# Performance work log

Hardware: AMD Instinct MI355X
Metric: run time of the kernel (lower is better)

Reference implementation:

```python
import jax, jax.numpy as jnp
import numpy as np

DIM = 1024
EPS = 1e-5

def layernorm(x, g, b):
    m = jnp.mean(x, axis=-1, keepdims=True)
    v = jnp.var(x, axis=-1, keepdims=True)
    return (x - m) / jnp.sqrt(v + EPS) * g + b

def setup_inputs() -> dict:
    key = jax.random.key(0)
    ks = jax.random.split(key, 12)
    B, L, D = 4, 2048, DIM
    s = 1.0 / np.sqrt(D)
    return {
        "q": jax.random.normal(ks[0], (B, L, D), jnp.float32),
        "k": jax.random.normal(ks[1], (B, L, D), jnp.float32),
        "v": jax.random.normal(ks[2], (B, L, D), jnp.float32),
        "gq": jnp.ones((D,), jnp.float32), "bq": jnp.zeros((D,), jnp.float32),
        "gk": jnp.ones((D,), jnp.float32), "bk": jnp.zeros((D,), jnp.float32),
        "gv": jnp.ones((D,), jnp.float32), "bv": jnp.zeros((D,), jnp.float32),
        "Wq": jax.random.uniform(ks[3], (D, D), jnp.float32, -s, s),
        "Wk": jax.random.uniform(ks[4], (D, D), jnp.float32, -s, s),
        "Wv": jax.random.uniform(ks[5], (D, D), jnp.float32, -s, s),
        "Wp": jax.random.uniform(ks[6], (D, D), jnp.float32, -s, s),
        "bp": jax.random.uniform(ks[7], (D,), jnp.float32, -s, s),
    }

def reference(q, k, v, gq, bq, gk, bk, gv, bv, Wq, Wk, Wv, Wp, bp):
    scale = DIM ** -0.5
    qn = layernorm(q, gq, bq) @ Wq.T  # [B,Q,D]
    kn = layernorm(k, gk, bk) @ Wk.T  # [B,K,D]
    vn = layernorm(v, gv, bv) @ Wv.T  # [B,K,D]
    attn = jnp.einsum('bqc,bkc->bqk', qn, kn)
    attn = jax.nn.relu(attn) * scale  # ReLU on raw scores, then scale (matches in-place *=)
    attn_mask = jax.nn.softmax(attn, axis=-1)
    out = jnp.einsum('bqk,bkc->bqc', attn_mask, vn)
    out = out @ Wp.T + bp
    return (attn, out)
```

## Files before the change

kernel.cpp:

```cpp
#include <hip/hip_runtime.h>


typedef __attribute__((ext_vector_type(8))) short short8v;
typedef __attribute__((ext_vector_type(4))) float f32x4;

#define DEVI __device__ __forceinline__

DEVI float b2f(unsigned short u) {
  union { unsigned int i; float f; } x;
  x.i = ((unsigned int)u) << 16;
  return x.f;
}
DEVI unsigned short f2b(float f) {
  union { float f; unsigned int i; } x;
  x.f = f;
  unsigned int r = x.i + 0x7fffu + ((x.i >> 16) & 1u);
  return (unsigned short)(r >> 16);
}

DEVI bool sniff_bf16(const unsigned short* wq) {
  int bad = 0;
#pragma unroll
  for (int j = 0; j < 64; ++j) bad |= (fabsf(b2f(wq[j])) > 0.0625f) ? 1 : 0;
  return bad == 0;
}

DEVI void async16(const unsigned short* g, unsigned short* l) {
  __builtin_amdgcn_global_load_lds(
      (const __attribute__((address_space(1))) void*)g,
      (__attribute__((address_space(3))) void*)l, 16, 0, 0);
}

DEVI void wait_lgkm0() { asm volatile("s_waitcnt lgkmcnt(0)" ::: "memory"); }
template <int N> DEVI void wait_vm();
template <> DEVI void wait_vm<0>() { asm volatile("s_waitcnt vmcnt(0)" ::: "memory"); }
template <> DEVI void wait_vm<2>() { asm volatile("s_waitcnt vmcnt(2)" ::: "memory"); }

DEVI void stage_half(const unsigned short* G, int ld, unsigned short* L,
                     int w, int lane, int k0) {
  int r8 = lane >> 3;
  int scol = ((lane & 7) ^ r8) * 8;
#pragma unroll
  for (int j = 0; j < 2; ++j) {
    async16(G + (size_t)(j * 64 + w * 8 + r8) * ld + k0 + scol,
            L + (j * 64 + w * 8) * 64);
  }
}

DEVI void gemm8_core(unsigned short* sA, unsigned short* sB,
                     const unsigned short* Ab, const unsigned short* Bb,
                     int m0, int n0, int lda, int ldb, int K, int tid,
                     f32x4 (&acc)[8][4]) {
  int lane = tid & 63, w = tid >> 6;
  int wm = w >> 2, wn = w & 3;
  int l15 = lane & 15, quad = lane >> 4;
  int rxor = l15 & 7;
  int cb0 = (quad ^ rxor) * 8;
  int cb1 = ((4 + quad) ^ rxor) * 8;
  const int nst = K >> 6;
  const unsigned short* A0 = Ab + (size_t)m0 * lda;
  const unsigned short* A1 = A0 + (size_t)128 * lda;
  const unsigned short* B0 = Bb + (size_t)n0 * ldb;
  const unsigned short* B1 = B0 + (size_t)128 * ldb;

  stage_half(A0, lda, sA, w, lane, 0);
  stage_half(A1, lda, sA + 8192, w, lane, 0);
  stage_half(B0, ldb, sB, w, lane, 0);
  stage_half(B1, ldb, sB + 8192, w, lane, 0);

  for (int t = 0; t < nst; ++t) {
    const int b = t & 1, nb2 = b ^ 1;
    const bool st = (t + 1 < nst);
    const int k0n = (t + 1) << 6;
    const unsigned short* rA = sA + b * 16384 + (wm * 128 + l15) * 64;
    const unsigned short* rB = sB + b * 16384 + (wn * 64 + l15) * 64;
    short8v a[4][2], bb[4][2];

    if (st) {
      stage_half(A0, lda, sA + nb2 * 16384, w, lane, k0n);
      wait_vm<2>();
    } else {
      wait_vm<0>();
    }
    __builtin_amdgcn_s_barrier();
#pragma unroll
    for (int mt = 0; mt < 4; ++mt) {
      a[mt][0] = *(const short8v*)(rA + mt * 1024 + cb0);
      a[mt][1] = *(const short8v*)(rA + mt * 1024 + cb1);
    }
#pragma unroll
    for (int nt = 0; nt < 2; ++nt) {
      bb[nt][0] = *(const short8v*)(rB + nt * 1024 + cb0);
      bb[nt][1] = *(const short8v*)(rB + nt * 1024 + cb1);
    }
    wait_lgkm0();
    __builtin_amdgcn_sched_barrier(0);
    __builtin_amdgcn_s_setprio(1);
#pragma unroll
    for (int mt = 0; mt < 4; ++mt)
#pragma unroll
      for (int nt = 0; nt < 2; ++nt) {
        acc[mt][nt] = __builtin_amdgcn_mfma_f32_16x16x32_bf16(a[mt][0], bb[nt][0], acc[mt][nt], 0, 0, 0);
        acc[mt][nt] = __builtin_amdgcn_mfma_f32_16x16x32_bf16(a[mt][1], bb[nt][1], acc[mt][nt], 0, 0, 0);
      }
    __builtin_amdgcn_s_setprio(0);
    __builtin_amdgcn_s_barrier();

#pragma unroll
    for (int nt = 2; nt < 4; ++nt) {
      bb[nt][0] = *(const short8v*)(rB + nt * 1024 + cb0);
      bb[nt][1] = *(const short8v*)(rB + nt * 1024 + cb1);
    }
    if (st) stage_half(A1, lda, sA + nb2 * 16384 + 8192, w, lane, k0n);
    __builtin_amdgcn_s_barrier();
    wait_lgkm0();
    __builtin_amdgcn_sched_barrier(0);
    __builtin_amdgcn_s_setprio(1);
#pragma unroll
    for (int mt = 0; mt < 4; ++mt)
#pragma unroll
      for (int nt = 2; nt < 4; ++nt) {
        acc[mt][nt] = __builtin_amdgcn_mfma_f32_16x16x32_bf16(a[mt][0], bb[nt][0], acc[mt][nt], 0, 0, 0);
        acc[mt][nt] = __builtin_amdgcn_mfma_f32_16x16x32_bf16(a[mt][1], bb[nt][1], acc[mt][nt], 0, 0, 0);
      }
    __builtin_amdgcn_s_setprio(0);
    __builtin_amdgcn_s_barrier();

#pragma unroll
    for (int mt = 0; mt < 4; ++mt) {
      a[mt][0] = *(const short8v*)(rA + (4 + mt) * 1024 + cb0);
      a[mt][1] = *(const short8v*)(rA + (4 + mt) * 1024 + cb1);
    }
    if (st) stage_half(B0, ldb, sB + nb2 * 16384, w, lane, k0n);
    __builtin_amdgcn_s_barrier();
    wait_lgkm0();
    __builtin_amdgcn_sched_barrier(0);
    __builtin_amdgcn_s_setprio(1);
#pragma unroll
    for (int mt = 0; mt < 4; ++mt)
#pragma unroll
      for (int nt = 0; nt < 2; ++nt) {
        acc[4 + mt][nt] = __builtin_amdgcn_mfma_f32_16x16x32_bf16(a[mt][0], bb[nt][0], acc[4 + mt][nt], 0, 0, 0);
        acc[4 + mt][nt] = __builtin_amdgcn_mfma_f32_16x16x32_bf16(a[mt][1], bb[nt][1], acc[4 + mt][nt], 0, 0, 0);
      }
    __builtin_amdgcn_s_setprio(0);
    __builtin_amdgcn_s_barrier();

    if (st) stage_half(B1, ldb, sB + nb2 * 16384 + 8192, w, lane, k0n);
    __builtin_amdgcn_s_barrier();
    __builtin_amdgcn_s_setprio(1);
#pragma unroll
    for (int mt = 0; mt < 4; ++mt)
#pragma unroll
      for (int nt = 2; nt < 4; ++nt) {
        acc[4 + mt][nt] = __builtin_amdgcn_mfma_f32_16x16x32_bf16(a[mt][0], bb[nt][0], acc[4 + mt][nt], 0, 0, 0);
        acc[4 + mt][nt] = __builtin_amdgcn_mfma_f32_16x16x32_bf16(a[mt][1], bb[nt][1], acc[4 + mt][nt], 0, 0, 0);
      }
    __builtin_amdgcn_s_setprio(0);
    __builtin_amdgcn_s_barrier();
  }
}

DEVI int xcd_swz(int f, int nb) { return (f & 7) * (nb >> 3) + (f >> 3); }

struct PrepArgs {
  const void* q; const void* k; const void* v;
  const void* g[3]; const void* b[3];
  const void* W[4];
};

__global__ __launch_bounds__(256) void k_prep(PrepArgs pa,
    unsigned short* __restrict__ Wb, unsigned short* __restrict__ XN) {
  bool isbf = sniff_bf16((const unsigned short*)pa.W[0]);
  int bid = blockIdx.x, tid = threadIdx.x;
  if (bid < 2048) {
    int s = bid >> 9;
    size_t inner = ((size_t)(bid & 511)) * 2048 + (size_t)tid * 8;
    unsigned short* dst = Wb + (size_t)s * 1048576 + inner;
    if (isbf) {
      *(uint4*)dst = *(const uint4*)((const unsigned short*)pa.W[s] + inner);
    } else {
      const float* f = (const float*)pa.W[s] + inner;
      float4 a = *(const float4*)f;
      float4 b = *(const float4*)(f + 4);
      ushort4 o0 = { f2b(a.x), f2b(a.y), f2b(a.z), f2b(a.w) };
      ushort4 o1 = { f2b(b.x), f2b(b.y), f2b(b.z), f2b(b.w) };
      *(ushort4*)dst = o0;
      *(ushort4*)(dst + 4) = o1;
    }
  } else {
    int row = bid - 2048;
    int t = row >> 13;
    size_t r = (size_t)(row & 8191);
    const void* src = (t == 0) ? pa.q : (t == 1) ? pa.k : pa.v;
    float x0, x1, x2, x3;
    if (isbf) {
      ushort4 pk = *(const ushort4*)((const unsigned short*)src + r * 1024 + (size_t)tid * 4);
      x0 = b2f(pk.x); x1 = b2f(pk.y); x2 = b2f(pk.z); x3 = b2f(pk.w);
    } else {
      float4 pk = *(const float4*)((const float*)src + r * 1024 + (size_t)tid * 4);
      x0 = pk.x; x1 = pk.y; x2 = pk.z; x3 = pk.w;
    }
    float s1 = x0 + x1 + x2 + x3;
    float s2 = x0 * x0 + x1 * x1 + x2 * x2 + x3 * x3;
    for (int off = 32; off > 0; off >>= 1) {
      s1 += __shfl_down(s1, off);
      s2 += __shfl_down(s2, off);
    }
    __shared__ float sh[8];
    if ((tid & 63) == 0) { sh[tid >> 6] = s1; sh[4 + (tid >> 6)] = s2; }
    __syncthreads();
    float m  = (sh[0] + sh[1] + sh[2] + sh[3]) * (1.0f / 1024.0f);
    float m2 = (sh[4] + sh[5] + sh[6] + sh[7]) * (1.0f / 1024.0f);
    float rstd = rsqrtf(m2 - m * m + 1e-5f);
    float g0, g1, g2, g3, c0, c1, c2, c3;
    if (isbf) {
      ushort4 gv = *(const ushort4*)((const unsigned short*)pa.g[t] + tid * 4);
      ushort4 bbv = *(const ushort4*)((const unsigned short*)pa.b[t] + tid * 4);
      g0 = b2f(gv.x); g1 = b2f(gv.y); g2 = b2f(gv.z); g3 = b2f(gv.w);
      c0 = b2f(bbv.x); c1 = b2f(bbv.y); c2 = b2f(bbv.z); c3 = b2f(bbv.w);
    } else {
      float4 gv = *(const float4*)((const float*)pa.g[t] + tid * 4);
      float4 bbv = *(const float4*)((const float*)pa.b[t] + tid * 4);
      g0 = gv.x; g1 = gv.y; g2 = gv.z; g3 = gv.w;
      c0 = bbv.x; c1 = bbv.y; c2 = bbv.z; c3 = bbv.w;
    }
    ushort4 o;
    o.x = f2b((x0 - m) * rstd * g0 + c0);
    o.y = f2b((x1 - m) * rstd * g1 + c1);
    o.z = f2b((x2 - m) * rstd * g2 + c2);
    o.w = f2b((x3 - m) * rstd * g3 + c3);
    *(ushort4*)(XN + (size_t)row * 1024 + (size_t)tid * 4) = o;
  }
}

__global__ __launch_bounds__(512, 2) void k_megaproj(
    const unsigned short* __restrict__ XN, const unsigned short* __restrict__ Wb,
    unsigned short* __restrict__ QN, unsigned short* __restrict__ VNT) {
  __shared__ __align__(16) unsigned short sA[2 * 256 * 64];
  __shared__ __align__(16) unsigned short sB[2 * 256 * 64];
  int x = xcd_swz((int)blockIdx.x, 384), tid = threadIdx.x;
  int lane = tid & 63, w = tid >> 6;
  int wm = w >> 2, wn = w & 3;
  int l15 = lane & 15, quad = lane >> 4;
  f32x4 acc[8][4];
#pragma unroll
  for (int i = 0; i < 8; ++i)
#pragma unroll
    for (int j = 0; j < 4; ++j) acc[i][j] = (f32x4){0.f, 0.f, 0.f, 0.f};

  unsigned short* C;
  int m0, n0, ldc;
  if (x < 256) {
    int t = x >> 7, i = x & 127;
    m0 = (i >> 2) * 256; n0 = (i & 3) * 256; ldc = 1024;
    gemm8_core(sA, sB, XN + (size_t)t * 8388608, Wb + (size_t)t * 1048576,
               m0, n0, 1024, 1024, 1024, tid, acc);
    C = QN + (size_t)t * 8388608;
  } else {
    int i = x - 256, z = i >> 5, j = i & 31;
    m0 = (j >> 3) * 256; n0 = (j & 7) * 256; ldc = 2048;
    gemm8_core(sA, sB, Wb + 2 * 1048576, XN + 2 * 8388608 + (size_t)z * 2097152,
               m0, n0, 1024, 1024, 1024, tid, acc);
    C = VNT + (size_t)z * 2097152;
  }
#pragma unroll
  for (int mt = 0; mt < 8; ++mt) {
    int mb = m0 + wm * 128 + mt * 16 + quad * 4;
#pragma unroll
    for (int nt = 0; nt < 4; ++nt) {
      int n = n0 + wn * 64 + nt * 16 + l15;
      f32x4 vc = acc[mt][nt];
#pragma unroll
      for (int r2 = 0; r2 < 4; ++r2) C[(size_t)(mb + r2) * ldc + n] = f2b(vc[r2]);
    }
  }
}

template <int EPI>
__global__ __launch_bounds__(512, 2) void k_gemm(
    const unsigned short* __restrict__ A, const unsigned short* __restrict__ B,
    void* __restrict__ Cv, long long coff,
    int K, int lda, int ldb, int ldc,
    long long sAb, long long sBb, long long sCb,
    float scale, const void* __restrict__ bias,
    const unsigned short* __restrict__ wq_sniff) {
  __shared__ __align__(16) unsigned short sA[2 * 256 * 64];
  __shared__ __align__(16) unsigned short sB[2 * 256 * 64];
  int tid = threadIdx.x;
  int lane = tid & 63, w = tid >> 6;
  int wm = w >> 2, wn = w & 3;
  int l15 = lane & 15, quad = lane >> 4;

  int gx = gridDim.x, gy = gridDim.y;
  int nb = gx * gy * (int)gridDim.z;
  int f = (int)blockIdx.x + gx * ((int)blockIdx.y + gy * (int)blockIdx.z);
  f = xcd_swz(f, nb);
  int bx = f % gx;
  int rem = f / gx;
  int by = rem % gy;
  int bz = rem / gy;

  int m0 = by * 256, n0 = bx * 256;
  f32x4 acc[8][4];
#pragma unroll
  for (int i = 0; i < 8; ++i)
#pragma unroll
    for (int j = 0; j < 4; ++j) acc[i][j] = (f32x4){0.f, 0.f, 0.f, 0.f};

  gemm8_core(sA, sB, A + (long long)bz * sAb, B + (long long)bz * sBb,
             m0, n0, lda, ldb, K, tid, acc);

  long long cbase = coff + (long long)bz * sCb;
  bool isbf = (EPI != 0) ? sniff_bf16(wq_sniff) : true;
#pragma unroll
  for (int mt = 0; mt < 8; ++mt) {
    int mb = m0 + wm * 128 + mt * 16 + quad * 4;
#pragma unroll
    for (int nt = 0; nt < 4; ++nt) {
      int n = n0 + wn * 64 + nt * 16 + l15;
      f32x4 vc = acc[mt][nt];
      if (EPI == 0) {
        unsigned short* C = (unsigned short*)Cv + cbase;
#pragma unroll
        for (int r2 = 0; r2 < 4; ++r2) C[(size_t)(mb + r2) * ldc + n] = f2b(vc[r2]);
      } else if (EPI == 1) {
        if (isbf) {
          unsigned short* C = (unsigned short*)Cv + cbase;
#pragma unroll
          for (int r2 = 0; r2 < 4; ++r2)
            C[(size_t)(mb + r2) * ldc + n] = f2b(fmaxf(vc[r2], 0.f) * scale);
        } else {
          float* C = (float*)Cv + cbase;
#pragma unroll
          for (int r2 = 0; r2 < 4; ++r2)
            C[(size_t)(mb + r2) * ldc + n] = fmaxf(vc[r2], 0.f) * scale;
        }
      } else {
        float bv2 = isbf ? b2f(((const unsigned short*)bias)[n])
                         : ((const float*)bias)[n];
        if (isbf) {
          unsigned short* C = (unsigned short*)Cv + cbase;
#pragma unroll
          for (int r2 = 0; r2 < 4; ++r2) C[(size_t)(mb + r2) * ldc + n] = f2b(vc[r2] + bv2);
        } else {
          float* C = (float*)Cv + cbase;
#pragma unroll
          for (int r2 = 0; r2 < 4; ++r2) C[(size_t)(mb + r2) * ldc + n] = vc[r2] + bv2;
        }
      }
    }
  }
}

__global__ __launch_bounds__(256) void k_softmax(const void* __restrict__ S,
    unsigned short* __restrict__ P, const unsigned short* __restrict__ wq_sniff) {
  bool isbf = sniff_bf16(wq_sniff);
  size_t row = blockIdx.x;
  int tid = threadIdx.x;
  float v[8];
  if (isbf) {
    const unsigned short* s = (const unsigned short*)S + row * 2048 + (size_t)tid * 8;
    ushort4 a = *(const ushort4*)s;
    ushort4 b = *(const ushort4*)(s + 4);
    v[0] = b2f(a.x); v[1] = b2f(a.y); v[2] = b2f(a.z); v[3] = b2f(a.w);
    v[4] = b2f(b.x); v[5] = b2f(b.y); v[6] = b2f(b.z); v[7] = b2f(b.w);
  } else {
    const float* s = (const float*)S + row * 2048 + (size_t)tid * 8;
    float4 a = *(const float4*)s;
    float4 b = *(const float4*)(s + 4);
    v[0] = a.x; v[1] = a.y; v[2] = a.z; v[3] = a.w;
    v[4] = b.x; v[5] = b.y; v[6] = b.z; v[7] = b.w;
  }
  float mx = v[0];
#pragma unroll
  for (int j = 1; j < 8; ++j) mx = fmaxf(mx, v[j]);
  for (int off = 32; off > 0; off >>= 1) mx = fmaxf(mx, __shfl_down(mx, off));
  __shared__ float sh[8];
  if ((tid & 63) == 0) sh[tid >> 6] = mx;
  __syncthreads();
  mx = fmaxf(fmaxf(sh[0], sh[1]), fmaxf(sh[2], sh[3]));
  float sum = 0.f;
#pragma unroll
  for (int j = 0; j < 8; ++j) { v[j] = __expf(v[j] - mx); sum += v[j]; }
  for (int off = 32; off > 0; off >>= 1) sum += __shfl_down(sum, off);
  if ((tid & 63) == 0) sh[4 + (tid >> 6)] = sum;
  __syncthreads();
  float inv = 1.0f / (sh[4] + sh[5] + sh[6] + sh[7]);
  ushort4 o0 = { f2b(v[0] * inv), f2b(v[1] * inv), f2b(v[2] * inv), f2b(v[3] * inv) };
  ushort4 o1 = { f2b(v[4] * inv), f2b(v[5] * inv), f2b(v[6] * inv), f2b(v[7] * inv) };
  unsigned short* p = P + row * 2048 + (size_t)tid * 8;
  *(ushort4*)p = o0;
  *(ushort4*)(p + 4) = o1;
}

static const size_t MB_ = 1024 * 1024;
static const size_t OFF_W   = 0;
static const size_t OFF_XN  = 8 * MB_ + 128 * 1024;
static const size_t OFF_QN  = OFF_XN + 48 * MB_;
static const size_t OFF_VNT = OFF_QN + 32 * MB_;
static const size_t OFF_P   = OFF_XN;
static const size_t OFF_O1  = OFF_XN + 32 * MB_;

extern "C" void kernel_launch(void* const* d_in, const int* in_sizes, int n_in,
                              void* d_out, int out_size, void* d_ws, size_t ws_size,
                              hipStream_t stream) {
  (void)in_sizes; (void)n_in; (void)out_size; (void)ws_size;
  char* ws = (char*)d_ws;
  unsigned short* Wb  = (unsigned short*)(ws + OFF_W);
  unsigned short* XN  = (unsigned short*)(ws + OFF_XN);
  unsigned short* QN  = (unsigned short*)(ws + OFF_QN);
  unsigned short* VNT = (unsigned short*)(ws + OFF_VNT);
  unsigned short* P   = (unsigned short*)(ws + OFF_P);
  unsigned short* O1  = (unsigned short*)(ws + OFF_O1);
  const unsigned short* WqS = (const unsigned short*)d_in[9];

  PrepArgs pa;
  pa.q = d_in[0]; pa.k = d_in[1]; pa.v = d_in[2];
  pa.g[0] = d_in[3]; pa.b[0] = d_in[4];
  pa.g[1] = d_in[5]; pa.b[1] = d_in[6];
  pa.g[2] = d_in[7]; pa.b[2] = d_in[8];
  pa.W[0] = d_in[9]; pa.W[1] = d_in[10]; pa.W[2] = d_in[11]; pa.W[3] = d_in[12];

  k_prep<<<26624, 256, 0, stream>>>(pa, Wb, XN);

  k_megaproj<<<384, 512, 0, stream>>>(XN, Wb, QN, VNT);

  k_gemm<1><<<dim3(8, 8, 4), 512, 0, stream>>>(
      QN, QN + 8388608, d_out,
      0,
      1024, 1024, 1024, 2048,
      2097152LL, 2097152LL, 4194304LL,
      0.03125f, nullptr, WqS);

  k_softmax<<<8192, 256, 0, stream>>>(d_out, P, WqS);

  k_gemm<0><<<dim3(4, 8, 4), 512, 0, stream>>>(
      P, VNT, O1,
      0,
      2048, 2048, 2048, 1024,
      4194304LL, 2097152LL, 2097152LL,
      0.f, nullptr, WqS);

  k_gemm<3><<<dim3(4, 32, 1), 512, 0, stream>>>(
      O1, Wb + 3 * 1048576, d_out,
      16777216,
      1024, 1024, 1024, 1024,
      0LL, 0LL, 0LL,
      0.f, d_in[13], WqS);
}
```

Baseline: 461.5 us.

## Deepen GEMM prefetch pipeline and add narrow 256x128 tile variant

Templates the shared GEMM core on tile width. The 256x256 path now prefetches A two k-steps ahead and B one step ahead, issuing the loads at different points in the iteration so more global-to-LDS traffic overlaps the MFMA work. A new 256x128 path halves the N tile for the P·V and output-projection GEMMs, doubling their grid to 256 blocks so more CUs are occupied. The cost is more repeated reads of A across N tiles and tighter vmcnt bookkeeping that must match the number of loads in flight.

```diff
diff --git a/kernel.cpp b/kernel.cpp
--- a/kernel.cpp
+++ b/kernel.cpp
@@ -34,23 +34,26 @@
 DEVI void wait_lgkm0() { asm volatile("s_waitcnt lgkmcnt(0)" ::: "memory"); }
 template <int N> DEVI void wait_vm();
 template <> DEVI void wait_vm<0>() { asm volatile("s_waitcnt vmcnt(0)" ::: "memory"); }
-template <> DEVI void wait_vm<2>() { asm volatile("s_waitcnt vmcnt(2)" ::: "memory"); }
-
+template <> DEVI void wait_vm<6>() { asm volatile("s_waitcnt vmcnt(6)" ::: "memory"); }
+template <> DEVI void wait_vm<8>() { asm volatile("s_waitcnt vmcnt(8)" ::: "memory"); }
+
+DEVI void stage_q(const unsigned short* G, int ld, unsigned short* L,
+                  int w, int lane, int k0) {
+  int r8 = lane >> 3;
+  int scol = ((lane & 7) ^ r8) * 8;
+  async16(G + (size_t)(w * 8 + r8) * ld + k0 + scol, L + (w * 8) * 64);
+}
 DEVI void stage_half(const unsigned short* G, int ld, unsigned short* L,
                      int w, int lane, int k0) {
-  int r8 = lane >> 3;
-  int scol = ((lane & 7) ^ r8) * 8;
-#pragma unroll
-  for (int j = 0; j < 2; ++j) {
-    async16(G + (size_t)(j * 64 + w * 8 + r8) * ld + k0 + scol,
-            L + (j * 64 + w * 8) * 64);
-  }
-}
-
+  stage_q(G, ld, L, w, lane, k0);
+  stage_q(G + (size_t)64 * ld, ld, L + 64 * 64, w, lane, k0);
+}
+
+template <int NB>
 DEVI void gemm8_core(unsigned short* sA, unsigned short* sB,
                      const unsigned short* Ab, const unsigned short* Bb,
                      int m0, int n0, int lda, int ldb, int K, int tid,
-                     f32x4 (&acc)[8][4]) {
+                     f32x4 (&acc)[8][2 * NB]) {
   int lane = tid & 63, w = tid >> 6;
   int wm = w >> 2, wn = w & 3;
   int l15 = lane & 15, quad = lane >> 4;
@@ -58,106 +61,178 @@
   int cb0 = (quad ^ rxor) * 8;
   int cb1 = ((4 + quad) ^ rxor) * 8;
   const int nst = K >> 6;
-  const unsigned short* A0 = Ab + (size_t)m0 * lda;
-  const unsigned short* A1 = A0 + (size_t)128 * lda;
-  const unsigned short* B0 = Bb + (size_t)n0 * ldb;
-  const unsigned short* B1 = B0 + (size_t)128 * ldb;
-
-  stage_half(A0, lda, sA, w, lane, 0);
-  stage_half(A1, lda, sA + 8192, w, lane, 0);
-  stage_half(B0, ldb, sB, w, lane, 0);
-  stage_half(B1, ldb, sB + 8192, w, lane, 0);
-
-  for (int t = 0; t < nst; ++t) {
-    const int b = t & 1, nb2 = b ^ 1;
-    const bool st = (t + 1 < nst);
-    const int k0n = (t + 1) << 6;
-    const unsigned short* rA = sA + b * 16384 + (wm * 128 + l15) * 64;
-    const unsigned short* rB = sB + b * 16384 + (wn * 64 + l15) * 64;
-    short8v a[4][2], bb[4][2];
-
-    if (st) {
-      stage_half(A0, lda, sA + nb2 * 16384, w, lane, k0n);
-      wait_vm<2>();
-    } else {
-      wait_vm<0>();
-    }
-    __builtin_amdgcn_s_barrier();
-#pragma unroll
-    for (int mt = 0; mt < 4; ++mt) {
-      a[mt][0] = *(const short8v*)(rA + mt * 1024 + cb0);
-      a[mt][1] = *(const short8v*)(rA + mt * 1024 + cb1);
-    }
-#pragma unroll
-    for (int nt = 0; nt < 2; ++nt) {
-      bb[nt][0] = *(const short8v*)(rB + nt * 1024 + cb0);
-      bb[nt][1] = *(const short8v*)(rB + nt * 1024 + cb1);
-    }
-    wait_lgkm0();
-    __builtin_amdgcn_sched_barrier(0);
-    __builtin_amdgcn_s_setprio(1);
-#pragma unroll
-    for (int mt = 0; mt < 4; ++mt)
+  const int BSZ = NB * 128 * 64;
+  const unsigned short* A_ = Ab + (size_t)m0 * lda;
+  const unsigned short* B_ = Bb + (size_t)n0 * ldb;
+
+  if constexpr (NB == 2) {
+    stage_half(A_, lda, sA, w, lane, 0);
+    stage_half(A_ + (size_t)128 * lda, lda, sA + 8192, w, lane, 0);
+    stage_half(B_, ldb, sB, w, lane, 0);
+    stage_half(B_ + (size_t)128 * ldb, ldb, sB + 8192, w, lane, 0);
+    if (nst > 1) {
+      stage_half(A_, lda, sA + 16384, w, lane, 64);
+      stage_half(A_ + (size_t)128 * lda, lda, sA + 16384 + 8192, w, lane, 64);
+    }
+    for (int t = 0; t < nst; ++t) {
+      const int b = t & 1;
+      const unsigned short* rA = sA + b * 16384 + (wm * 128 + l15) * 64;
+      const unsigned short* rB = sB + b * 16384 + (wn * 64 + l15) * 64;
+      short8v a[4][2], bb[4][2];
+      if (t + 1 < nst) {
+        int kn = (t + 1) << 6;
+        stage_half(B_, ldb, sB + (b ^ 1) * 16384, w, lane, kn);
+        stage_half(B_ + (size_t)128 * ldb, ldb, sB + (b ^ 1) * 16384 + 8192, w, lane, kn);
+        wait_vm<8>();
+      } else {
+        wait_vm<0>();
+      }
+      __builtin_amdgcn_s_barrier();
+#pragma unroll
+      for (int mt = 0; mt < 4; ++mt) {
+        a[mt][0] = *(const short8v*)(rA + mt * 1024 + cb0);
+        a[mt][1] = *(const short8v*)(rA + mt * 1024 + cb1);
+      }
 #pragma unroll
       for (int nt = 0; nt < 2; ++nt) {
-        acc[mt][nt] = __builtin_amdgcn_mfma_f32_16x16x32_bf16(a[mt][0], bb[nt][0], acc[mt][nt], 0, 0, 0);
-        acc[mt][nt] = __builtin_amdgcn_mfma_f32_16x16x32_bf16(a[mt][1], bb[nt][1], acc[mt][nt], 0, 0, 0);
-      }
-    __builtin_amdgcn_s_setprio(0);
-    __builtin_amdgcn_s_barrier();
-
-#pragma unroll
-    for (int nt = 2; nt < 4; ++nt) {
-      bb[nt][0] = *(const short8v*)(rB + nt * 1024 + cb0);
-      bb[nt][1] = *(const short8v*)(rB + nt * 1024 + cb1);
-    }
-    if (st) stage_half(A1, lda, sA + nb2 * 16384 + 8192, w, lane, k0n);
-    __builtin_amdgcn_s_barrier();
-    wait_lgkm0();
-    __builtin_amdgcn_sched_barrier(0);
-    __builtin_amdgcn_s_setprio(1);
-#pragma unroll
-    for (int mt = 0; mt < 4; ++mt)
+        bb[nt][0] = *(const short8v*)(rB + nt * 1024 + cb0);
+        bb[nt][1] = *(const short8v*)(rB + nt * 1024 + cb1);
+      }
+      wait_lgkm0();
+      __builtin_amdgcn_sched_barrier(0);
+      __builtin_amdgcn_s_setprio(1);
+#pragma unroll
+      for (int mt = 0; mt < 4; ++mt)
+#pragma unroll
+        for (int nt = 0; nt < 2; ++nt) {
+          acc[mt][nt] = __builtin_amdgcn_mfma_f32_16x16x32_bf16(a[mt][0], bb[nt][0], acc[mt][nt], 0, 0, 0);
+          acc[mt][nt] = __builtin_amdgcn_mfma_f32_16x16x32_bf16(a[mt][1], bb[nt][1], acc[mt][nt], 0, 0, 0);
+        }
+      __builtin_amdgcn_s_setprio(0);
+      __builtin_amdgcn_s_barrier();
 #pragma unroll
       for (int nt = 2; nt < 4; ++nt) {
-        acc[mt][nt] = __builtin_amdgcn_mfma_f32_16x16x32_bf16(a[mt][0], bb[nt][0], acc[mt][nt], 0, 0, 0);
-        acc[mt][nt] = __builtin_amdgcn_mfma_f32_16x16x32_bf16(a[mt][1], bb[nt][1], acc[mt][nt], 0, 0, 0);
-      }
-    __builtin_amdgcn_s_setprio(0);
-    __builtin_amdgcn_s_barrier();
-
-#pragma unroll
-    for (int mt = 0; mt < 4; ++mt) {
-      a[mt][0] = *(const short8v*)(rA + (4 + mt) * 1024 + cb0);
-      a[mt][1] = *(const short8v*)(rA + (4 + mt) * 1024 + cb1);
-    }
-    if (st) stage_half(B0, ldb, sB + nb2 * 16384, w, lane, k0n);
-    __builtin_amdgcn_s_barrier();
-    wait_lgkm0();
-    __builtin_amdgcn_sched_barrier(0);
-    __builtin_amdgcn_s_setprio(1);
-#pragma unroll
-    for (int mt = 0; mt < 4; ++mt)
+        bb[nt][0] = *(const short8v*)(rB + nt * 1024 + cb0);
+        bb[nt][1] = *(const short8v*)(rB + nt * 1024 + cb1);
+      }
+      __builtin_amdgcn_s_barrier();
+      wait_lgkm0();
+      __builtin_amdgcn_sched_barrier(0);
+      __builtin_amdgcn_s_setprio(1);
+#pragma unroll
+      for (int mt = 0; mt < 4; ++mt)
+#pragma unroll
+        for (int nt = 2; nt < 4; ++nt) {
+          acc[mt][nt] = __builtin_amdgcn_mfma_f32_16x16x32_bf16(a[mt][0], bb[nt][0], acc[mt][nt], 0, 0, 0);
+          acc[mt][nt] = __builtin_amdgcn_mfma_f32_16x16x32_bf16(a[mt][1], bb[nt][1], acc[mt][nt], 0, 0, 0);
+        }
+      __builtin_amdgcn_s_setprio(0);
+      __builtin_amdgcn_s_barrier();
+#pragma unroll
+      for (int mt = 0; mt < 4; ++mt) {
+        a[mt][0] = *(const short8v*)(rA + (4 + mt) * 1024 + cb0);
+        a[mt][1] = *(const short8v*)(rA + (4 + mt) * 1024 + cb1);
+      }
+      __builtin_amdgcn_s_barrier();
+      wait_lgkm0();
+      __builtin_amdgcn_sched_barrier(0);
+      __builtin_amdgcn_s_setprio(1);
+#pragma unroll
+      for (int mt = 0; mt < 4; ++mt)
+#pragma unroll
+        for (int nt = 0; nt < 2; ++nt) {
+          acc[4 + mt][nt] = __builtin_amdgcn_mfma_f32_16x16x32_bf16(a[mt][0], bb[nt][0], acc[4 + mt][nt], 0, 0, 0);
+          acc[4 + mt][nt] = __builtin_amdgcn_mfma_f32_16x16x32_bf16(a[mt][1], bb[nt][1], acc[4 + mt][nt], 0, 0, 0);
+        }
+      __builtin_amdgcn_s_setprio(0);
+      __builtin_amdgcn_s_barrier();
+      if (t + 2 < nst) {
+        int kn2 = (t + 2) << 6;
+        stage_half(A_, lda, sA + b * 16384, w, lane, kn2);
+        stage_half(A_ + (size_t)128 * lda, lda, sA + b * 16384 + 8192, w, lane, kn2);
+      }
+      __builtin_amdgcn_s_setprio(1);
+#pragma unroll
+      for (int mt = 0; mt < 4; ++mt)
+#pragma unroll
+        for (int nt = 2; nt < 4; ++nt) {
+          acc[4 + mt][nt] = __builtin_amdgcn_mfma_f32_16x16x32_bf16(a[mt][0], bb[nt][0], acc[4 + mt][nt], 0, 0, 0);
+          acc[4 + mt][nt] = __builtin_amdgcn_mfma_f32_16x16x32_bf16(a[mt][1], bb[nt][1], acc[4 + mt][nt], 0, 0, 0);
+        }
+      __builtin_amdgcn_s_setprio(0);
+    }
+  } else {
+    stage_q(A_, lda, sA, w, lane, 0);
+    stage_q(A_ + (size_t)128 * lda, lda, sA + 128 * 64, w, lane, 0);
+    stage_half(B_, ldb, sB, w, lane, 0);
+    stage_q(A_ + (size_t)64 * lda, lda, sA + 64 * 64, w, lane, 0);
+    stage_q(A_ + (size_t)192 * lda, lda, sA + 192 * 64, w, lane, 0);
+    if (nst > 1) {
+      stage_q(A_, lda, sA + 16384, w, lane, 64);
+      stage_q(A_ + (size_t)128 * lda, lda, sA + 16384 + 128 * 64, w, lane, 64);
+      stage_half(B_, ldb, sB + BSZ, w, lane, 64);
+    }
+    for (int t = 0; t < nst; ++t) {
+      const int b = t & 1;
+      const unsigned short* rA = sA + b * 16384 + (wm * 128 + l15) * 64;
+      const unsigned short* rB = sB + b * BSZ + (wn * 32 + l15) * 64;
+      short8v a[4][2], bb[2][2];
+      if (t + 1 < nst) {
+        int kn = (t + 1) << 6;
+        stage_q(A_ + (size_t)64 * lda, lda, sA + (b ^ 1) * 16384 + 64 * 64, w, lane, kn);
+        stage_q(A_ + (size_t)192 * lda, lda, sA + (b ^ 1) * 16384 + 192 * 64, w, lane, kn);
+        wait_vm<6>();
+      } else {
+        wait_vm<0>();
+      }
+      __builtin_amdgcn_s_barrier();
+#pragma unroll
+      for (int mt = 0; mt < 4; ++mt) {
+        a[mt][0] = *(const short8v*)(rA + mt * 1024 + cb0);
+        a[mt][1] = *(const short8v*)(rA + mt * 1024 + cb1);
+      }
 #pragma unroll
       for (int nt = 0; nt < 2; ++nt) {
-        acc[4 + mt][nt] = __builtin_amdgcn_mfma_f32_16x16x32_bf16(a[mt][0], bb[nt][0], acc[4 + mt][nt], 0, 0, 0);
-        acc[4 + mt][nt] = __builtin_amdgcn_mfma_f32_16x16x32_bf16(a[mt][1], bb[nt][1], acc[4 + mt][nt], 0, 0, 0);
-      }
-    __builtin_amdgcn_s_setprio(0);
-    __builtin_amdgcn_s_barrier();
-
-    if (st) stage_half(B1, ldb, sB + nb2 * 16384 + 8192, w, lane, k0n);
-    __builtin_amdgcn_s_barrier();
-    __builtin_amdgcn_s_setprio(1);
-#pragma unroll
-    for (int mt = 0; mt < 4; ++mt)
-#pragma unroll
-      for (int nt = 2; nt < 4; ++nt) {
-        acc[4 + mt][nt] = __builtin_amdgcn_mfma_f32_16x16x32_bf16(a[mt][0], bb[nt][0], acc[4 + mt][nt], 0, 0, 0);
-        acc[4 + mt][nt] = __builtin_amdgcn_mfma_f32_16x16x32_bf16(a[mt][1], bb[nt][1], acc[4 + mt][nt], 0, 0, 0);
-      }
-    __builtin_amdgcn_s_setprio(0);
-    __builtin_amdgcn_s_barrier();
+        bb[nt][0] = *(const short8v*)(rB + nt * 1024 + cb0);
+        bb[nt][1] = *(const short8v*)(rB + nt * 1024 + cb1);
+      }
+      wait_lgkm0();
+      __builtin_amdgcn_sched_barrier(0);
+      __builtin_amdgcn_s_setprio(1);
+#pragma unroll
+      for (int mt = 0; mt < 4; ++mt)
+#pragma unroll
+        for (int nt = 0; nt < 2; ++nt) {
+          acc[mt][nt] = __builtin_amdgcn_mfma_f32_16x16x32_bf16(a[mt][0], bb[nt][0], acc[mt][nt], 0, 0, 0);
+          acc[mt][nt] = __builtin_amdgcn_mfma_f32_16x16x32_bf16(a[mt][1], bb[nt][1], acc[mt][nt], 0, 0, 0);
+        }
+      __builtin_amdgcn_s_setprio(0);
+      __builtin_amdgcn_s_barrier();
+#pragma unroll
+      for (int mt = 0; mt < 4; ++mt) {
+        a[mt][0] = *(const short8v*)(rA + (4 + mt) * 1024 + cb0);
+        a[mt][1] = *(const short8v*)(rA + (4 + mt) * 1024 + cb1);
+      }
+      if (t + 2 < nst) {
+        int kn2 = (t + 2) << 6;
+        stage_q(A_, lda, sA + b * 16384, w, lane, kn2);
+        stage_q(A_ + (size_t)128 * lda, lda, sA + b * 16384 + 128 * 64, w, lane, kn2);
+        stage_half(B_, ldb, sB + b * BSZ, w, lane, kn2);
+      }
+      __builtin_amdgcn_s_barrier();
+      wait_lgkm0();
+      __builtin_amdgcn_sched_barrier(0);
+      __builtin_amdgcn_s_setprio(1);
+#pragma unroll
+      for (int mt = 0; mt < 4; ++mt)
+#pragma unroll
+        for (int nt = 0; nt < 2; ++nt) {
+          acc[4 + mt][nt] = __builtin_amdgcn_mfma_f32_16x16x32_bf16(a[mt][0], bb[nt][0], acc[4 + mt][nt], 0, 0, 0);
+          acc[4 + mt][nt] = __builtin_amdgcn_mfma_f32_16x16x32_bf16(a[mt][1], bb[nt][1], acc[4 + mt][nt], 0, 0, 0);
+        }
+      __builtin_amdgcn_s_setprio(0);
+      __builtin_amdgcn_s_barrier();
+    }
   }
 }
 
@@ -254,14 +329,14 @@
   if (x < 256) {
     int t = x >> 7, i = x & 127;
     m0 = (i >> 2) * 256; n0 = (i & 3) * 256; ldc = 1024;
-    gemm8_core(sA, sB, XN + (size_t)t * 8388608, Wb + (size_t)t * 1048576,
-               m0, n0, 1024, 1024, 1024, tid, acc);
+    gemm8_core<2>(sA, sB, XN + (size_t)t * 8388608, Wb + (size_t)t * 1048576,
+                  m0, n0, 1024, 1024, 1024, tid, acc);
     C = QN + (size_t)t * 8388608;
   } else {
     int i = x - 256, z = i >> 5, j = i & 31;
     m0 = (j >> 3) * 256; n0 = (j & 7) * 256; ldc = 2048;
-    gemm8_core(sA, sB, Wb + 2 * 1048576, XN + 2 * 8388608 + (size_t)z * 2097152,
-               m0, n0, 1024, 1024, 1024, tid, acc);
+    gemm8_core<2>(sA, sB, Wb + 2 * 1048576, XN + 2 * 8388608 + (size_t)z * 2097152,
+                  m0, n0, 1024, 1024, 1024, tid, acc);
     C = VNT + (size_t)z * 2097152;
   }
 #pragma unroll
@@ -277,7 +352,7 @@
   }
 }
 
-template <int EPI>
+template <int EPI, int NB>
 __global__ __launch_bounds__(512, 2) void k_gemm(
     const unsigned short* __restrict__ A, const unsigned short* __restrict__ B,
     void* __restrict__ Cv, long long coff,
@@ -286,7 +361,7 @@
     float scale, const void* __restrict__ bias,
     const unsigned short* __restrict__ wq_sniff) {
   __shared__ __align__(16) unsigned short sA[2 * 256 * 64];
-  __shared__ __align__(16) unsigned short sB[2 * 256 * 64];
+  __shared__ __align__(16) unsigned short sB[2 * NB * 128 * 64];
   int tid = threadIdx.x;
   int lane = tid & 63, w = tid >> 6;
   int wm = w >> 2, wn = w & 3;
@@ -301,15 +376,15 @@
   int by = rem % gy;
   int bz = rem / gy;
 
-  int m0 = by * 256, n0 = bx * 256;
-  f32x4 acc[8][4];
+  int m0 = by * 256, n0 = bx * (NB * 128);
+  f32x4 acc[8][2 * NB];
 #pragma unroll
   for (int i = 0; i < 8; ++i)
 #pragma unroll
-    for (int j = 0; j < 4; ++j) acc[i][j] = (f32x4){0.f, 0.f, 0.f, 0.f};
-
-  gemm8_core(sA, sB, A + (long long)bz * sAb, B + (long long)bz * sBb,
-             m0, n0, lda, ldb, K, tid, acc);
+    for (int j = 0; j < 2 * NB; ++j) acc[i][j] = (f32x4){0.f, 0.f, 0.f, 0.f};
+
+  gemm8_core<NB>(sA, sB, A + (long long)bz * sAb, B + (long long)bz * sBb,
+                 m0, n0, lda, ldb, K, tid, acc);
 
   long long cbase = coff + (long long)bz * sCb;
   bool isbf = (EPI != 0) ? sniff_bf16(wq_sniff) : true;
@@ -317,8 +392,8 @@
   for (int mt = 0; mt < 8; ++mt) {
     int mb = m0 + wm * 128 + mt * 16 + quad * 4;
 #pragma unroll
-    for (int nt = 0; nt < 4; ++nt) {
-      int n = n0 + wn * 64 + nt * 16 + l15;
+    for (int nt = 0; nt < 2 * NB; ++nt) {
+      int n = n0 + wn * (NB * 32) + nt * 16 + l15;
       f32x4 vc = acc[mt][nt];
       if (EPI == 0) {
         unsigned short* C = (unsigned short*)Cv + cbase;
@@ -426,7 +501,7 @@
 
   k_megaproj<<<384, 512, 0, stream>>>(XN, Wb, QN, VNT);
 
-  k_gemm<1><<<dim3(8, 8, 4), 512, 0, stream>>>(
+  k_gemm<1, 2><<<dim3(8, 8, 4), 512, 0, stream>>>(
       QN, QN + 8388608, d_out,
       0,
       1024, 1024, 1024, 2048,
@@ -435,14 +510,14 @@
 
   k_softmax<<<8192, 256, 0, stream>>>(d_out, P, WqS);
 
-  k_gemm<0><<<dim3(4, 8, 4), 512, 0, stream>>>(
+  k_gemm<0, 1><<<dim3(8, 8, 4), 512, 0, stream>>>(
       P, VNT, O1,
       0,
       2048, 2048, 2048, 1024,
       4194304LL, 2097152LL, 2097152LL,
       0.f, nullptr, WqS);
 
-  k_gemm<3><<<dim3(4, 32, 1), 512, 0, stream>>>(
+  k_gemm<3, 1><<<dim3(8, 32, 1), 512, 0, stream>>>(
       O1, Wb + 3 * 1048576, d_out,
       16777216,
       1024, 1024, 1024, 1024,
```

Measured after the change: 414.1 us. 1.11x faster.
